# Optimization experiments

Hardware: AMD Instinct MI355X
Metric: run time of the kernel (lower is better)

## Reference

```python
import jax, jax.numpy as jnp
import numpy as np

B, K, D = 4, 2048, 512   # batch, time window (self._K), d_model
H, Q, V = 8, 64, 64      # heads, per-head query dim, per-head value dim


def setup_inputs() -> dict:
    key = jax.random.key(0)
    ks = jax.random.split(key, 10)
    s = 0.05
    return {
        "query": jax.random.normal(ks[0], (B, K, D), jnp.float32),
        "key":   jax.random.normal(ks[1], (B, K, D), jnp.float32),
        "value": jax.random.normal(ks[2], (B, K, D), jnp.float32),
        # stacked per-head Linear params (torch Linear: y = x W^T + b -> store as [h, D, out])
        "W_q": jax.random.normal(ks[3], (H, D, Q), jnp.float32) * s,
        "b_q": jax.random.normal(ks[4], (H, Q), jnp.float32) * s,
        "W_k": jax.random.normal(ks[5], (H, D, Q), jnp.float32) * s,
        "b_k": jax.random.normal(ks[6], (H, Q), jnp.float32) * s,
        "W_v": jax.random.normal(ks[7], (H, D, V), jnp.float32) * s,
        "b_v": jax.random.normal(ks[8], (H, V), jnp.float32) * s,
        "W_o": jax.random.normal(ks[9], (H * V, D), jnp.float32) * s,
        "b_o": jnp.zeros((D,), jnp.float32),
    }


def reference(query, key, value, W_q, b_q, W_k, b_k, W_v, b_v, W_o, b_o):
    # per-head projections, batched over heads: [B, H, K, Q/V]
    q = jnp.einsum("bkd,hdq->bhkq", query, W_q) + b_q[None, :, None, :]
    k = jnp.einsum("bkd,hdq->bhkq", key,   W_k) + b_k[None, :, None, :]
    v = jnp.einsum("bkd,hdv->bhkv", value, W_v) + b_v[None, :, None, :]
    # NOTE: original divides by sqrt(self._K) (time window), NOT sqrt(d_k)
    scores = jnp.einsum("bhkq,bhlq->bhkl", q, k) / np.sqrt(K).astype(np.float32)
    # mask == 'subsequent': causal triu mask above the diagonal
    causal = jnp.triu(jnp.ones((K, K), bool), k=1)
    scores = jnp.where(causal[None, None], -jnp.inf, scores)
    attn = jax.nn.softmax(scores, axis=-1)
    heads = jnp.einsum("bhkl,bhlv->bhkv", attn, v)          # [B, H, K, V]
    concat = heads.transpose(0, 2, 1, 3).reshape(B, K, H * V)  # concat along last dim
    return concat @ W_o + b_o
```

## Files before the change

### kernel.cpp

```cpp
#include <hip/hip_runtime.h>
#include <hip/hip_bf16.h>

typedef __attribute__((ext_vector_type(8))) short bf16x8;
typedef __attribute__((ext_vector_type(4))) float f32x4;

#define SEQ 2048
#define DM  512
#define NH  8
#define DH  64
#define QSCALE 0.031879360f

__device__ __forceinline__ unsigned short f2bf(float f) {
  unsigned int u = __float_as_uint(f);
  unsigned int r = 0x7FFFu + ((u >> 16) & 1u);
  return (unsigned short)((u + r) >> 16);
}

__device__ __forceinline__ void cvt8f(const float4& v0, const float4& v1,
                                      unsigned short* __restrict__ o) {
  o[0] = f2bf(v0.x); o[1] = f2bf(v0.y); o[2] = f2bf(v0.z); o[3] = f2bf(v0.w);
  o[4] = f2bf(v1.x); o[5] = f2bf(v1.y); o[6] = f2bf(v1.z); o[7] = f2bf(v1.w);
}

__device__ __forceinline__ void load8f(const float* __restrict__ s,
                                       unsigned short* __restrict__ o) {
  float4 v0 = *(const float4*)s;
  float4 v1 = *(const float4*)(s + 4);
  cvt8f(v0, v1, o);
}

__device__ __forceinline__ void gload16(const unsigned short* g, unsigned short* l) {
  __builtin_amdgcn_global_load_lds(
      (const __attribute__((address_space(1))) void*)g,
      (__attribute__((address_space(3))) void*)l, 16, 0, 0);
}

__global__ __launch_bounds__(256) void weight_prep(const float* __restrict__ Wq,
                                                   const float* __restrict__ Wk,
                                                   const float* __restrict__ Wv,
                                                   const float* __restrict__ Wo,
                                                   const float* __restrict__ q,
                                                   const float* __restrict__ k,
                                                   const float* __restrict__ v,
                                                   unsigned short* __restrict__ Wqt,
                                                   unsigned short* __restrict__ Wkt,
                                                   unsigned short* __restrict__ Wvt,
                                                   unsigned short* __restrict__ Wot,
                                                   unsigned short* __restrict__ Xb) {
  const int tid = threadIdx.x;
  if (blockIdx.x >= 256) {
    const int wi = blockIdx.x - 256;
    const float* src = (wi < 128) ? q : (wi < 256) ? k : v;
    const size_t off = (size_t)(wi & 127) * 32768;
    const float* s = src + off;
    unsigned short* d = Xb + (size_t)(wi >> 7) * (4u * SEQ * DM) + off;
#pragma unroll
    for (int i = 0; i < 16; ++i) {
      const size_t idx = (size_t)(tid + 256 * i) * 8;
      __align__(16) unsigned short t[8];
      load8f(s + idx, t);
      *(uint4*)(d + idx) = *(const uint4*)t;
    }
    return;
  }
  const int which = blockIdx.x >> 6, wi = blockIdx.x & 63;
  const float* src;
  unsigned short* dst;
  int R, C, r0, c0;
  if (which < 3) {
    const float* W = (which == 0) ? Wq : (which == 1) ? Wk : Wv;
    unsigned short* D = (which == 0) ? Wqt : (which == 1) ? Wkt : Wvt;
    int h = wi >> 3;
    src = W + (size_t)h * 512 * 64;
    dst = D + (size_t)h * 64 * 512;
    R = 512; C = 64; r0 = (wi & 7) * 64; c0 = 0;
  } else {
    src = Wo; dst = Wot;
    R = 512; C = 512; r0 = (wi >> 3) * 64; c0 = (wi & 7) * 64;
  }
  __shared__ __align__(16) unsigned short T[64][72];
#pragma unroll
  for (int i = 0; i < 2; ++i) {
    int c = tid + 256 * i;
    int lr = c >> 3, lc = (c & 7) * 8;
    __align__(16) unsigned short tmp[8];
    load8f(src + (size_t)(r0 + lr) * C + c0 + lc, tmp);
    *(uint4*)&T[lr][lc] = *(const uint4*)tmp;
  }
  __syncthreads();
#pragma unroll
  for (int i = 0; i < 2; ++i) {
    int c = tid + 256 * i;
    int orow = c >> 3, och = (c & 7) * 8;
    __align__(16) unsigned short tmp[8];
#pragma unroll
    for (int j = 0; j < 8; ++j) tmp[j] = T[och + j][orow];
    *(uint4*)(dst + (size_t)(c0 + orow) * R + r0 + och) = *(uint4*)tmp;
  }
}

__global__ __launch_bounds__(256, 4) void proj128(const unsigned short* __restrict__ Xb,
                                                  const unsigned short* __restrict__ Wqt,
                                                  const unsigned short* __restrict__ Wkt,
                                                  const unsigned short* __restrict__ Wvt,
                                                  const float* __restrict__ bq,
                                                  const float* __restrict__ bk,
                                                  const float* __restrict__ bv,
                                                  unsigned short* __restrict__ Qp,
                                                  unsigned short* __restrict__ Kp,
                                                  unsigned short* __restrict__ Vpt) {
  const int which = blockIdx.z;
  const unsigned short* X = Xb + (size_t)which * (4u * SEQ * DM);
  const unsigned short* Wt = (which == 0) ? Wqt : (which == 1) ? Wkt : Wvt;
  const float* bias = (which == 0) ? bq : (which == 1) ? bk : bv;
  unsigned short* out = (which == 0) ? Qp : (which == 1) ? Kp : Vpt;
  const float ps = (which == 0) ? QSCALE : 1.0f;

  const int m0 = blockIdx.x * 128;
  const int n0 = blockIdx.y * 128;
  __shared__ __align__(16) unsigned short smem[18432];
  const int tid  = threadIdx.x;
  const int wave = tid >> 6, lane = tid & 63;
  const int l15  = lane & 15, quad = lane >> 4;
  const int rb = (wave >> 1) * 64, cb = (wave & 1) * 64;

  const int srow = wave * 8 + (lane >> 3);
  const int g8   = (((lane & 7) ^ (lane >> 3)) << 3);
  const unsigned short* aSrc = X  + (size_t)(m0 + srow) * DM + g8;
  const unsigned short* bSrc = Wt + (size_t)(n0 + srow) * DM + g8;
  unsigned short* aDst = smem        + wave * 512 + lane * 8;
  unsigned short* bDst = smem + 8192 + wave * 512 + lane * 8;

  f32x4 acc[4][4];
#pragma unroll
  for (int i = 0; i < 4; ++i)
#pragma unroll
    for (int f = 0; f < 4; ++f) acc[i][f] = (f32x4){0.f, 0.f, 0.f, 0.f};

  for (int k0 = 0; k0 < DM; k0 += 64) {
    __syncthreads();
#pragma unroll
    for (int i = 0; i < 4; ++i) {
      gload16(aSrc + (size_t)(i * 32) * DM + k0, aDst + i * 2048);
      gload16(bSrc + (size_t)(i * 32) * DM + k0, bDst + i * 2048);
    }
    __syncthreads();
#pragma unroll
    for (int kc = 0; kc < 2; ++kc) {
      bf16x8 av[4], bv4[4];
#pragma unroll
      for (int i = 0; i < 4; ++i)
        av[i]  = *(const bf16x8*)(smem + (size_t)(rb + 16 * i + l15) * 64 +
                                  (((kc * 4 + quad) ^ (l15 & 7)) << 3));
#pragma unroll
      for (int f = 0; f < 4; ++f)
        bv4[f] = *(const bf16x8*)(smem + 8192 + (size_t)(cb + 16 * f + l15) * 64 +
                                  (((kc * 4 + quad) ^ (l15 & 7)) << 3));
#pragma unroll
      for (int i = 0; i < 4; ++i)
#pragma unroll
        for (int f = 0; f < 4; ++f)
          acc[i][f] = __builtin_amdgcn_mfma_f32_16x16x32_bf16(av[i], bv4[f], acc[i][f], 0, 0, 0);
    }
  }

  if (which < 2) {
#pragma unroll
    for (int i = 0; i < 4; ++i)
#pragma unroll
      for (int f = 0; f < 4; ++f)
#pragma unroll
        for (int r = 0; r < 4; ++r) {
          int m = m0 + rb + 16 * i + quad * 4 + r;
          int col = n0 + cb + 16 * f + l15;
          int head = col >> 6, o = col & 63;
          int b = m >> 11, s = m & (SEQ - 1);
          float val = (acc[i][f][r] + bias[col]) * ps;
          out[(((size_t)(b * NH + head) * SEQ + s) << 6) + o] = f2bf(val);
        }
  } else {
    __syncthreads();
    unsigned short* T = smem + wave * 4608;
#pragma unroll
    for (int i = 0; i < 4; ++i)
#pragma unroll
      for (int f = 0; f < 4; ++f)
#pragma unroll
        for (int r = 0; r < 4; ++r) {
          int lrow = 16 * i + quad * 4 + r;
          int lcol = 16 * f + l15;
          int col = n0 + cb + 16 * f + l15;
          T[lcol * 72 + lrow] = f2bf(acc[i][f][r] + bias[col]);
        }
    const int mbase = m0 + rb;
    const int b = mbase >> 11, sbase = mbase & (SEQ - 1);
    const int head = (n0 + cb) >> 6;
    unsigned short* dstb = out + ((size_t)(b * NH + head) * DH) * SEQ + sbase;
#pragma unroll
    for (int j = 0; j < 8; ++j) {
      int dh = (lane >> 3) + j * 8;
      int sc = (lane & 7) * 8;
      *(uint4*)(dstb + (size_t)dh * SEQ + sc) = *(const uint4*)&T[dh * 72 + sc];
    }
  }
}

__global__ __launch_bounds__(256, 4) void attn_kernel(const unsigned short* __restrict__ Qp,
                                                      const unsigned short* __restrict__ Kp,
                                                      const unsigned short* __restrict__ Vpt,
                                                      unsigned short* __restrict__ concat) {
  const int bh = blockIdx.x;
  const int ip = blockIdx.y;
  const int b = bh >> 3, h = bh & 7;
  const int qa = ip, qb = 31 - ip;
  __shared__ __align__(16) unsigned short Ks[2][64][72], Vts[2][64][72];
  const int tid  = threadIdx.x;
  const int wave = tid >> 6, lane = tid & 63;
  const int l15  = lane & 15, quad = lane >> 4;
  const int sub  = wave & 1;
  const bool isB = wave < 2;
  const int qt   = isB ? qb : qa;
  const unsigned short* Qb = Qp  + (size_t)bh * SEQ * DH;
  const unsigned short* Kb = Kp  + (size_t)bh * SEQ * DH;
  const unsigned short* Vb = Vpt + (size_t)bh * DH * SEQ;

  bf16x8 aq[2][2];
#pragma unroll
  for (int hb = 0; hb < 2; ++hb)
#pragma unroll
    for (int kc = 0; kc < 2; ++kc)
      aq[hb][kc] = *(const bf16x8*)(Qb + (size_t)(qt * 64 + sub * 32 + hb * 16 + l15) * DH +
                                    kc * 32 + quad * 8);

  float l_acc[2] = {0.f, 0.f};
  f32x4 Of[2][4];
#pragma unroll
  for (int hb = 0; hb < 2; ++hb)
#pragma unroll
    for (int f = 0; f < 4; ++f) Of[hb][f] = (f32x4){0.f, 0.f, 0.f, 0.f};

  const int sr = tid >> 3, sc = (tid & 7) * 8;
  uint4 kst0, kst1, vst0, vst1;

#define STAGE_LOAD(lt_) do {                                                   \
    kst0 = *(const uint4*)(Kb + (size_t)((lt_) * 64 + sr) * DH + sc);          \
    kst1 = *(const uint4*)(Kb + (size_t)((lt_) * 64 + sr + 32) * DH + sc);     \
    vst0 = *(const uint4*)(Vb + (size_t)sr * SEQ + (lt_) * 64 + sc);           \
    vst1 = *(const uint4*)(Vb + (size_t)(sr + 32) * SEQ + (lt_) * 64 + sc);    \
  } while (0)

#define STAGE_WRITE(bi_) do {                                                  \
    *(uint4*)&Ks[bi_][sr][sc]       = kst0;                                    \
    *(uint4*)&Ks[bi_][sr + 32][sc]  = kst1;                                    \
    *(uint4*)&Vts[bi_][sr][sc]      = vst0;                                    \
    *(uint4*)&Vts[bi_][sr + 32][sc] = vst1;                                    \
  } while (0)

#define CVTPK(d_, lo_, hi_) asm("v_cvt_pk_bf16_f32 %0, %1, %2" : "=v"(d_) : "v"(lo_), "v"(hi_))
#define PL32SWAP(a_, b_) asm("v_permlane32_swap_b32 %0, %1" : "+v"(a_), "+v"(b_))
#define PL16SWAP(a_, b_) asm("v_permlane16_swap_b32 %0, %1" : "+v"(a_), "+v"(b_))

  STAGE_LOAD(0);
  STAGE_WRITE(0);
  STAGE_LOAD(1);
  __syncthreads();

#pragma unroll 1
  for (int lt = 0; lt <= qb; ++lt) {
    const int cur = lt & 1;
    if (lt < qb) STAGE_WRITE(cur ^ 1);
    if (lt + 2 <= qb) STAGE_LOAD(lt + 2);

    if (isB || lt <= qa) {
      f32x4 S[2][4];
#pragma unroll
      for (int hb = 0; hb < 2; ++hb)
#pragma unroll
        for (int f = 0; f < 4; ++f) S[hb][f] = (f32x4){0.f, 0.f, 0.f, 0.f};
#pragma unroll
      for (int kc = 0; kc < 2; ++kc) {
#pragma unroll
        for (int f = 0; f < 4; ++f) {
          bf16x8 bk = *(const bf16x8*)&Ks[cur][16 * f + l15][kc * 32 + quad * 8];
          S[0][f] = __builtin_amdgcn_mfma_f32_16x16x32_bf16(bk, aq[0][kc], S[0][f], 0, 0, 0);
          S[1][f] = __builtin_amdgcn_mfma_f32_16x16x32_bf16(bk, aq[1][kc], S[1][f], 0, 0, 0);
        }
      }
      if (lt == qt) {
#pragma unroll
        for (int hb = 0; hb < 2; ++hb) {
          const int qloc = sub * 32 + hb * 16 + l15;
#pragma unroll
          for (int f = 0; f < 4; ++f)
#pragma unroll
            for (int r = 0; r < 4; ++r)
              if (16 * f + 4 * quad + r > qloc) S[hb][f][r] = -1e30f;
        }
      }
      unsigned int P0[2][4], P1[2][4];
#pragma unroll
      for (int hb = 0; hb < 2; ++hb)
#pragma unroll
        for (int f = 0; f < 4; ++f) {
          float p0 = __builtin_amdgcn_exp2f(S[hb][f][0]);
          float p1 = __builtin_amdgcn_exp2f(S[hb][f][1]);
          float p2 = __builtin_amdgcn_exp2f(S[hb][f][2]);
          float p3 = __builtin_amdgcn_exp2f(S[hb][f][3]);
          l_acc[hb] += (p0 + p1) + (p2 + p3);
          CVTPK(P0[hb][f], p0, p1);
          CVTPK(P1[hb][f], p2, p3);
        }
#pragma unroll
      for (int kc = 0; kc < 2; ++kc) {
        union { unsigned int u[4]; bf16x8 v; } ap[2];
#pragma unroll
        for (int hb = 0; hb < 2; ++hb) {
          unsigned int x0 = P0[hb][2 * kc], y0 = P0[hb][2 * kc + 1];
          unsigned int x1 = P1[hb][2 * kc], y1 = P1[hb][2 * kc + 1];
          PL32SWAP(x0, y0); PL16SWAP(x0, y0);
          PL32SWAP(x1, y1); PL16SWAP(x1, y1);
          ap[hb].u[0] = x0; ap[hb].u[1] = x1; ap[hb].u[2] = y0; ap[hb].u[3] = y1;
        }
#pragma unroll
        for (int f = 0; f < 4; ++f) {
          bf16x8 bvv = *(const bf16x8*)&Vts[cur][16 * f + l15][kc * 32 + quad * 8];
          Of[0][f] = __builtin_amdgcn_mfma_f32_16x16x32_bf16(ap[0].v, bvv, Of[0][f], 0, 0, 0);
          Of[1][f] = __builtin_amdgcn_mfma_f32_16x16x32_bf16(ap[1].v, bvv, Of[1][f], 0, 0, 0);
        }
      }
    }
    __syncthreads();
  }
#undef STAGE_LOAD
#undef STAGE_WRITE
#undef CVTPK
#undef PL32SWAP
#undef PL16SWAP

#pragma unroll
  for (int hb = 0; hb < 2; ++hb) {
    l_acc[hb] += __shfl_xor(l_acc[hb], 16);
    l_acc[hb] += __shfl_xor(l_acc[hb], 32);
  }
#pragma unroll
  for (int hb = 0; hb < 2; ++hb) {
    float rl[4];
#pragma unroll
    for (int r = 0; r < 4; ++r) rl[r] = 1.0f / __shfl(l_acc[hb], quad * 4 + r);
#pragma unroll
    for (int f = 0; f < 4; ++f)
#pragma unroll
      for (int r = 0; r < 4; ++r) {
        const int row = qt * 64 + sub * 32 + hb * 16 + quad * 4 + r;
        const int col = h * DH + 16 * f + l15;
        concat[(size_t)(b * SEQ + row) * DM + col] = f2bf(Of[hb][f][r] * rl[r]);
      }
  }
}

__global__ __launch_bounds__(256, 2) void gemm_out(const unsigned short* __restrict__ A,
                                                   const unsigned short* __restrict__ Bt,
                                                   const float* __restrict__ bias,
                                                   float* __restrict__ out) {
  const int m0 = blockIdx.x * 64;
  const int nbase = blockIdx.y * 128;
  __shared__ __align__(16) unsigned short Bs[2][64][64];
  const int tid  = threadIdx.x;
  const int wave = tid >> 6, lane = tid & 63;
  const int l15  = lane & 15, quad = lane >> 4;

  bf16x8 afr[16];
  const unsigned short* arow = A + (size_t)(m0 + 16 * wave + l15) * DM;
#pragma unroll
  for (int k0i = 0; k0i < 8; ++k0i)
#pragma unroll
    for (int kc = 0; kc < 2; ++kc)
      afr[k0i * 2 + kc] = *(const bf16x8*)(arow + k0i * 64 + kc * 32 + quad * 8);

  const int srow = wave * 8 + (lane >> 3);
  const int g8   = (((lane & 7) ^ (lane >> 3)) << 3);
  unsigned short* bDst = &Bs[0][0][0] + wave * 512 + lane * 8;

#define G_STAGE(s_, bi_) do {                                                    \
    const int n0_ = nbase + ((s_) >> 3) * 64, k0_ = ((s_) & 7) * 64;             \
    _Pragma("unroll")                                                            \
    for (int i_ = 0; i_ < 2; ++i_)                                               \
      gload16(Bt + (size_t)(n0_ + i_ * 32 + srow) * DM + k0_ + g8,               \
              bDst + (bi_) * 4096 + i_ * 2048);                                  \
  } while (0)

  f32x4 acc[2][4];
#pragma unroll
  for (int nh = 0; nh < 2; ++nh)
#pragma unroll
    for (int f = 0; f < 4; ++f) acc[nh][f] = (f32x4){0.f, 0.f, 0.f, 0.f};

  G_STAGE(0, 0);
  __syncthreads();

#pragma unroll
  for (int s = 0; s < 16; ++s) {
    const int cur = s & 1;
    if (s < 15) G_STAGE(s + 1, cur ^ 1);
    const int nh = s >> 3;
#pragma unroll
    for (int kc = 0; kc < 2; ++kc)
#pragma unroll
      for (int f = 0; f < 4; ++f) {
        bf16x8 bfv = *(const bf16x8*)(&Bs[cur][0][0] + (size_t)(16 * f + l15) * 64 +
                                      (((kc * 4 + quad) ^ (l15 & 7)) << 3));
        acc[nh][f] = __builtin_amdgcn_mfma_f32_16x16x32_bf16(afr[(s & 7) * 2 + kc], bfv, acc[nh][f], 0, 0, 0);
      }
    __syncthreads();
  }
#undef G_STAGE

#pragma unroll
  for (int nh = 0; nh < 2; ++nh)
#pragma unroll
    for (int f = 0; f < 4; ++f)
#pragma unroll
      for (int r = 0; r < 4; ++r) {
        int row = 16 * wave + quad * 4 + r;
        int col = nbase + nh * 64 + 16 * f + l15;
        out[(size_t)(m0 + row) * DM + col] = acc[nh][f][r] + bias[col];
      }
}

extern "C" void kernel_launch(void* const* d_in, const int* in_sizes, int n_in,
                              void* d_out, int out_size, void* d_ws, size_t ws_size,
                              hipStream_t stream) {
  const float* query = (const float*)d_in[0];
  const float* key   = (const float*)d_in[1];
  const float* value = (const float*)d_in[2];
  const float* W_q   = (const float*)d_in[3];
  const float* b_q   = (const float*)d_in[4];
  const float* W_k   = (const float*)d_in[5];
  const float* b_k   = (const float*)d_in[6];
  const float* W_v   = (const float*)d_in[7];
  const float* b_v   = (const float*)d_in[8];
  const float* W_o   = (const float*)d_in[9];
  const float* b_o   = (const float*)d_in[10];
  float* out = (float*)d_out;

  char* ws = (char*)d_ws;
  unsigned short* Wqt    = (unsigned short*)(ws + 0);
  unsigned short* Wkt    = (unsigned short*)(ws + 524288);
  unsigned short* Wvt    = (unsigned short*)(ws + 1048576);
  unsigned short* Wot    = (unsigned short*)(ws + 1572864);
  unsigned short* Qp     = (unsigned short*)(ws + 2097152);
  unsigned short* Kp     = (unsigned short*)(ws + 10485760);
  unsigned short* Vpt    = (unsigned short*)(ws + 18874368);
  unsigned short* concat = (unsigned short*)(ws + 27262976);
  unsigned short* Xb     = (unsigned short*)(ws + 35651584);

  weight_prep<<<dim3(640), 256, 0, stream>>>(W_q, W_k, W_v, W_o, query, key, value,
                                             Wqt, Wkt, Wvt, Wot, Xb);

  proj128<<<dim3(64, 4, 3), 256, 0, stream>>>(Xb, Wqt, Wkt, Wvt,
                                              b_q, b_k, b_v, Qp, Kp, Vpt);

  attn_kernel<<<dim3(32, 16), 256, 0, stream>>>(Qp, Kp, Vpt, concat);

  gemm_out<<<dim3(128, 4), 256, 0, stream>>>(concat, Wot, b_o, out);
}
```

Before: 180.8 us.

## Load K/V fragments directly from global memory, dropping LDS staging and barriers

```diff
diff --git a/kernel.cpp b/kernel.cpp
--- a/kernel.cpp
+++ b/kernel.cpp
@@ -205,7 +205,7 @@
   }
 }
 
-__global__ __launch_bounds__(256, 4) void attn_kernel(const unsigned short* __restrict__ Qp,
+__global__ __launch_bounds__(256, 3) void attn_kernel(const unsigned short* __restrict__ Qp,
                                                       const unsigned short* __restrict__ Kp,
                                                       const unsigned short* __restrict__ Vpt,
                                                       unsigned short* __restrict__ concat) {
@@ -213,13 +213,11 @@
   const int ip = blockIdx.y;
   const int b = bh >> 3, h = bh & 7;
   const int qa = ip, qb = 31 - ip;
-  __shared__ __align__(16) unsigned short Ks[2][64][72], Vts[2][64][72];
   const int tid  = threadIdx.x;
   const int wave = tid >> 6, lane = tid & 63;
   const int l15  = lane & 15, quad = lane >> 4;
   const int sub  = wave & 1;
-  const bool isB = wave < 2;
-  const int qt   = isB ? qb : qa;
+  const int qt   = (wave < 2) ? qb : qa;
   const unsigned short* Qb = Qp  + (size_t)bh * SEQ * DH;
   const unsigned short* Kb = Kp  + (size_t)bh * SEQ * DH;
   const unsigned short* Vb = Vpt + (size_t)bh * DH * SEQ;
@@ -239,100 +237,80 @@
 #pragma unroll
     for (int f = 0; f < 4; ++f) Of[hb][f] = (f32x4){0.f, 0.f, 0.f, 0.f};
 
-  const int sr = tid >> 3, sc = (tid & 7) * 8;
-  uint4 kst0, kst1, vst0, vst1;
-
-#define STAGE_LOAD(lt_) do {                                                   \
-    kst0 = *(const uint4*)(Kb + (size_t)((lt_) * 64 + sr) * DH + sc);          \
-    kst1 = *(const uint4*)(Kb + (size_t)((lt_) * 64 + sr + 32) * DH + sc);     \
-    vst0 = *(const uint4*)(Vb + (size_t)sr * SEQ + (lt_) * 64 + sc);           \
-    vst1 = *(const uint4*)(Vb + (size_t)(sr + 32) * SEQ + (lt_) * 64 + sc);    \
-  } while (0)
-
-#define STAGE_WRITE(bi_) do {                                                  \
-    *(uint4*)&Ks[bi_][sr][sc]       = kst0;                                    \
-    *(uint4*)&Ks[bi_][sr + 32][sc]  = kst1;                                    \
-    *(uint4*)&Vts[bi_][sr][sc]      = vst0;                                    \
-    *(uint4*)&Vts[bi_][sr + 32][sc] = vst1;                                    \
-  } while (0)
-
 #define CVTPK(d_, lo_, hi_) asm("v_cvt_pk_bf16_f32 %0, %1, %2" : "=v"(d_) : "v"(lo_), "v"(hi_))
 #define PL32SWAP(a_, b_) asm("v_permlane32_swap_b32 %0, %1" : "+v"(a_), "+v"(b_))
 #define PL16SWAP(a_, b_) asm("v_permlane16_swap_b32 %0, %1" : "+v"(a_), "+v"(b_))
 
-  STAGE_LOAD(0);
-  STAGE_WRITE(0);
-  STAGE_LOAD(1);
-  __syncthreads();
-
 #pragma unroll 1
-  for (int lt = 0; lt <= qb; ++lt) {
-    const int cur = lt & 1;
-    if (lt < qb) STAGE_WRITE(cur ^ 1);
-    if (lt + 2 <= qb) STAGE_LOAD(lt + 2);
-
-    if (isB || lt <= qa) {
-      f32x4 S[2][4];
-#pragma unroll
-      for (int hb = 0; hb < 2; ++hb)
-#pragma unroll
-        for (int f = 0; f < 4; ++f) S[hb][f] = (f32x4){0.f, 0.f, 0.f, 0.f};
-#pragma unroll
-      for (int kc = 0; kc < 2; ++kc) {
-#pragma unroll
-        for (int f = 0; f < 4; ++f) {
-          bf16x8 bk = *(const bf16x8*)&Ks[cur][16 * f + l15][kc * 32 + quad * 8];
-          S[0][f] = __builtin_amdgcn_mfma_f32_16x16x32_bf16(bk, aq[0][kc], S[0][f], 0, 0, 0);
-          S[1][f] = __builtin_amdgcn_mfma_f32_16x16x32_bf16(bk, aq[1][kc], S[1][f], 0, 0, 0);
-        }
-      }
-      if (lt == qt) {
-#pragma unroll
-        for (int hb = 0; hb < 2; ++hb) {
-          const int qloc = sub * 32 + hb * 16 + l15;
-#pragma unroll
-          for (int f = 0; f < 4; ++f)
-#pragma unroll
-            for (int r = 0; r < 4; ++r)
-              if (16 * f + 4 * quad + r > qloc) S[hb][f][r] = -1e30f;
-        }
-      }
-      unsigned int P0[2][4], P1[2][4];
-#pragma unroll
-      for (int hb = 0; hb < 2; ++hb)
-#pragma unroll
-        for (int f = 0; f < 4; ++f) {
-          float p0 = __builtin_amdgcn_exp2f(S[hb][f][0]);
-          float p1 = __builtin_amdgcn_exp2f(S[hb][f][1]);
-          float p2 = __builtin_amdgcn_exp2f(S[hb][f][2]);
-          float p3 = __builtin_amdgcn_exp2f(S[hb][f][3]);
-          l_acc[hb] += (p0 + p1) + (p2 + p3);
-          CVTPK(P0[hb][f], p0, p1);
-          CVTPK(P1[hb][f], p2, p3);
-        }
-#pragma unroll
-      for (int kc = 0; kc < 2; ++kc) {
-        union { unsigned int u[4]; bf16x8 v; } ap[2];
-#pragma unroll
-        for (int hb = 0; hb < 2; ++hb) {
-          unsigned int x0 = P0[hb][2 * kc], y0 = P0[hb][2 * kc + 1];
-          unsigned int x1 = P1[hb][2 * kc], y1 = P1[hb][2 * kc + 1];
-          PL32SWAP(x0, y0); PL16SWAP(x0, y0);
-          PL32SWAP(x1, y1); PL16SWAP(x1, y1);
-          ap[hb].u[0] = x0; ap[hb].u[1] = x1; ap[hb].u[2] = y0; ap[hb].u[3] = y1;
-        }
-#pragma unroll
-        for (int f = 0; f < 4; ++f) {
-          bf16x8 bvv = *(const bf16x8*)&Vts[cur][16 * f + l15][kc * 32 + quad * 8];
-          Of[0][f] = __builtin_amdgcn_mfma_f32_16x16x32_bf16(ap[0].v, bvv, Of[0][f], 0, 0, 0);
-          Of[1][f] = __builtin_amdgcn_mfma_f32_16x16x32_bf16(ap[1].v, bvv, Of[1][f], 0, 0, 0);
-        }
-      }
-    }
-    __syncthreads();
-  }
-#undef STAGE_LOAD
-#undef STAGE_WRITE
+  for (int lt = 0; lt <= qt; ++lt) {
+    const int l0 = lt * 64;
+    bf16x8 vf[2][4];
+#pragma unroll
+    for (int kc = 0; kc < 2; ++kc)
+#pragma unroll
+      for (int f = 0; f < 4; ++f)
+        vf[kc][f] = *(const bf16x8*)(Vb + (size_t)(16 * f + l15) * SEQ + l0 + kc * 32 + quad * 8);
+
+    f32x4 S[2][4];
+#pragma unroll
+    for (int hb = 0; hb < 2; ++hb)
+#pragma unroll
+      for (int f = 0; f < 4; ++f) S[hb][f] = (f32x4){0.f, 0.f, 0.f, 0.f};
+    __builtin_amdgcn_s_setprio(1);
+#pragma unroll
+    for (int kc = 0; kc < 2; ++kc) {
+#pragma unroll
+      for (int f = 0; f < 4; ++f) {
+        bf16x8 bk = *(const bf16x8*)(Kb + (size_t)(l0 + 16 * f + l15) * DH + kc * 32 + quad * 8);
+        S[0][f] = __builtin_amdgcn_mfma_f32_16x16x32_bf16(bk, aq[0][kc], S[0][f], 0, 0, 0);
+        S[1][f] = __builtin_amdgcn_mfma_f32_16x16x32_bf16(bk, aq[1][kc], S[1][f], 0, 0, 0);
+      }
+    }
+    __builtin_amdgcn_s_setprio(0);
+    if (lt == qt) {
+#pragma unroll
+      for (int hb = 0; hb < 2; ++hb) {
+        const int qloc = sub * 32 + hb * 16 + l15;
+#pragma unroll
+        for (int f = 0; f < 4; ++f)
+#pragma unroll
+          for (int r = 0; r < 4; ++r)
+            if (16 * f + 4 * quad + r > qloc) S[hb][f][r] = -1e30f;
+      }
+    }
+    unsigned int P0[2][4], P1[2][4];
+#pragma unroll
+    for (int hb = 0; hb < 2; ++hb)
+#pragma unroll
+      for (int f = 0; f < 4; ++f) {
+        float p0 = __builtin_amdgcn_exp2f(S[hb][f][0]);
+        float p1 = __builtin_amdgcn_exp2f(S[hb][f][1]);
+        float p2 = __builtin_amdgcn_exp2f(S[hb][f][2]);
+        float p3 = __builtin_amdgcn_exp2f(S[hb][f][3]);
+        l_acc[hb] += (p0 + p1) + (p2 + p3);
+        CVTPK(P0[hb][f], p0, p1);
+        CVTPK(P1[hb][f], p2, p3);
+      }
+    __builtin_amdgcn_s_setprio(1);
+#pragma unroll
+    for (int kc = 0; kc < 2; ++kc) {
+      union { unsigned int u[4]; bf16x8 v; } ap[2];
+#pragma unroll
+      for (int hb = 0; hb < 2; ++hb) {
+        unsigned int x0 = P0[hb][2 * kc], y0 = P0[hb][2 * kc + 1];
+        unsigned int x1 = P1[hb][2 * kc], y1 = P1[hb][2 * kc + 1];
+        PL32SWAP(x0, y0); PL16SWAP(x0, y0);
+        PL32SWAP(x1, y1); PL16SWAP(x1, y1);
+        ap[hb].u[0] = x0; ap[hb].u[1] = x1; ap[hb].u[2] = y0; ap[hb].u[3] = y1;
+      }
+#pragma unroll
+      for (int f = 0; f < 4; ++f) {
+        Of[0][f] = __builtin_amdgcn_mfma_f32_16x16x32_bf16(ap[0].v, vf[kc][f], Of[0][f], 0, 0, 0);
+        Of[1][f] = __builtin_amdgcn_mfma_f32_16x16x32_bf16(ap[1].v, vf[kc][f], Of[1][f], 0, 0, 0);
+      }
+    }
+    __builtin_amdgcn_s_setprio(0);
+  }
 #undef CVTPK
 #undef PL32SWAP
 #undef PL16SWAP
```

Result: slower. 211.0 us (+16.7%).
